# Optimization experiments

Measured on AMD Instinct MI355X. Metric: run time of the kernel, lower is better.

The kernel has to match this reference:

```python
import jax, jax.numpy as jnp
import numpy as np

ALPHA = 0.2  # LeakyReLU negative slope
NEG_BIG = -9e15


def setup_inputs() -> dict:
    key = jax.random.key(0)
    k_h, k_adj, k_W, k_a = jax.random.split(key, 4)
    B, N, F_in, F_out = 8, 2048, 128, 64
    h = jax.random.normal(k_h, (B, N, F_in), dtype=jnp.float32)
    adj = jax.random.randint(k_adj, (B, N, N), 0, 2, dtype=jnp.int32)
    # xavier_uniform: bound = sqrt(6/(fan_in+fan_out))
    bW = float(np.sqrt(6.0 / (F_in + F_out)))
    W = jax.random.uniform(k_W, (F_in, F_out), dtype=jnp.float32, minval=-bW, maxval=bW)
    ba = float(np.sqrt(6.0 / (2 * F_out + 1)))
    a = jax.random.uniform(k_a, (2 * F_out, 1), dtype=jnp.float32, minval=-ba, maxval=ba)
    return {"h": h, "adj": adj, "W": W, "a": a}


def reference(h, adj, W, a):
    # h: [B,N,Fin], adj: [B,N,N], W: [Fin,Fout], a: [2*Fout,1]
    F_out = W.shape[1]
    Wh = jnp.einsum('bnf,fo->bno', h, W)               # [B,N,Fout]
    a1 = a[:F_out, 0]                                   # [Fout] (source/i part)
    a2 = a[F_out:, 0]                                   # [Fout] (target/j part)
    # e_ij = leakyrelu(Wh_i . a1 + Wh_j . a2) -- avoids O(N^2*2F) concat
    si = Wh @ a1                                        # [B,N]
    sj = Wh @ a2                                        # [B,N]
    e = si[:, :, None] + sj[:, None, :]                 # [B,N,N]
    e = jnp.where(e > 0, e, ALPHA * e)                  # LeakyReLU
    e = jnp.where(adj > 0, e, NEG_BIG)                  # mask non-edges
    attention = jax.nn.softmax(e, axis=2)               # [B,N,N]
    # dropout omitted (eval / training=False)
    h_prime = jnp.einsum('bij,bjo->bio', attention, Wh)  # [B,N,Fout]
    return h_prime
```

## Files before the change

### kernel.cpp

```cpp
#include <hip/hip_runtime.h>
#include <hip/hip_bf16.h>

#define ALPHA 0.2f
#define LOG2E 1.4426950408889634f

typedef __attribute__((ext_vector_type(8))) short bf16x8;
typedef __attribute__((ext_vector_type(4))) float f32x4;
typedef __attribute__((ext_vector_type(4))) int i32x4;

__device__ __forceinline__ int cvt_pk_bf16(float lo, float hi) {
    int r;
    asm("v_cvt_pk_bf16_f32 %0, %1, %2" : "=v"(r) : "v"(lo), "v"(hi));
    return r;
}

__device__ __forceinline__ void stage16(const void* g, void* l) {
    __builtin_amdgcn_global_load_lds(
        (const __attribute__((address_space(1))) void*)g,
        (__attribute__((address_space(3))) void*)l, 16, 0, 0);
}

__global__ __launch_bounds__(256) void gat_precompute(
    const float* __restrict__ h, const float* __restrict__ W,
    const float* __restrict__ a, unsigned short* __restrict__ WhT,
    float* __restrict__ si2, float* __restrict__ sj2)
{
    __shared__ float h_lds[32][128];
    __shared__ float wh_lds[32][65];
    const int tid  = threadIdx.x;
    const int lane = tid & 63;
    const int wave = tid >> 6;
    const long long row0 = (long long)blockIdx.x * 32;

    {
        const float4* s4 = (const float4*)(h + row0 * 128);
        #pragma unroll
        for (int i = 0; i < 4; ++i) {
            int idx = tid + i * 256;
            float4 v = s4[idx];
            *(float4*)&h_lds[idx >> 5][(idx & 31) * 4] = v;
        }
    }
    __syncthreads();

    const float a1 = a[lane];
    const float a2 = a[64 + lane];
    float acc[8];
    #pragma unroll
    for (int r = 0; r < 8; ++r) acc[r] = 0.0f;

    for (int f = 0; f < 128; f += 4) {
        const float w0 = W[(f+0)*64 + lane];
        const float w1 = W[(f+1)*64 + lane];
        const float w2 = W[(f+2)*64 + lane];
        const float w3 = W[(f+3)*64 + lane];
        #pragma unroll
        for (int r = 0; r < 8; ++r) {
            const float4 hv = *(const float4*)&h_lds[wave*8 + r][f];
            acc[r] = fmaf(hv.x, w0, acc[r]);
            acc[r] = fmaf(hv.y, w1, acc[r]);
            acc[r] = fmaf(hv.z, w2, acc[r]);
            acc[r] = fmaf(hv.w, w3, acc[r]);
        }
    }

    #pragma unroll
    for (int r = 0; r < 8; ++r) {
        const int rr = wave*8 + r;
        wh_lds[rr][lane] = acc[r];
        float s1 = acc[r] * a1;
        float s2 = acc[r] * a2;
        #pragma unroll
        for (int off = 32; off > 0; off >>= 1) {
            s1 += __shfl_xor(s1, off);
            s2 += __shfl_xor(s2, off);
        }
        if (lane == 0) {
            si2[row0 + rr] = s1 * LOG2E;
            sj2[row0 + rr] = s2 * LOG2E;
        }
    }
    __syncthreads();

    const long long b  = row0 >> 11;
    const int n0 = (int)(row0 & 2047);
    const int o  = tid >> 2;
    const int c0 = (tid & 3) * 8;
    i32x4 pk;
    #pragma unroll
    for (int k = 0; k < 4; ++k)
        pk[k] = cvt_pk_bf16(wh_lds[c0 + 2*k][o], wh_lds[c0 + 2*k + 1][o]);
    *(i32x4*)(WhT + (b*64 + o)*2048 + n0 + c0) = pk;
}

__global__ __launch_bounds__(256) void gat_attention(
    const int* __restrict__ adj, const unsigned short* __restrict__ WhT,
    const float* __restrict__ si2, const float* __restrict__ sj2,
    float* __restrict__ out)
{
    __shared__ char ldsbuf[65536];
    const int tid  = threadIdx.x;
    const int lane = tid & 63;
    const int wave = tid >> 6;
    const int bid  = blockIdx.x;
    const int b    = bid >> 6;
    const int i0   = (bid & 63) << 5;
    const int arow = lane & 15;
    const int g    = lane >> 4;
    const int half = wave >> 1;
    const int rgrp = wave & 1;
    const long long bN = (long long)b * 2048;

    const int* asrc[4];
    #pragma unroll
    for (int rd = 0; rd < 4; ++rd) {
        int U = (wave*4 + rd)*64 + lane;
        int r = U >> 5, pu = U & 31;
        int u = pu ^ (r & 15);
        int col = (u < 16) ? u*4 : (1024 + (u-16)*4);
        asrc[rd] = adj + (bN + i0 + r)*2048 + col;
    }
    const unsigned short* wsrc[4];
    #pragma unroll
    for (int rd = 0; rd < 4; ++rd) {
        int U  = wave*256 + rd*64 + lane;
        int hf = U >> 9;
        int o  = (U & 511) >> 3;
        int pu = U & 7;
        wsrc[rd] = WhT + ((long long)b*64 + o)*2048 + hf*1024
                       + ((pu ^ (o & 7)) * 8);
    }

    const float* sjb = sj2 + bN;
    float mx = -INFINITY;
    #pragma unroll 4
    for (int i = 0; i < 32; ++i) mx = fmaxf(mx, sjb[lane + i*64]);
    #pragma unroll
    for (int off = 32; off > 0; off >>= 1) mx = fmaxf(mx, __shfl_xor(mx, off));

    const float si_r = si2[bN + i0 + rgrp*16 + arow];
    const float u0f  = si_r + mx;
    const float m2   = fmaxf(u0f, ALPHA * u0f);
    const float Ci   = si_r - m2;
    const float Di   = ALPHA * si_r - m2;
    const int   rr   = rgrp*16 + arow;

    f32x4 accf[4];
    #pragma unroll
    for (int ob = 0; ob < 4; ++ob) accf[ob] = (f32x4){0.f,0.f,0.f,0.f};
    f32x4 accl = (f32x4){0.f,0.f,0.f,0.f};
    bf16x8 ones;
    #pragma unroll
    for (int k = 0; k < 8; ++k) ones[k] = (short)0x3F80;

    #define STAGE(S, STEP) { \
        const int ja = (STEP) * 64; \
        char* ab_ = ldsbuf + (S)*32768; \
        stage16(asrc[0] + ja, ab_ + (wave*4+0)*1024); \
        stage16(asrc[1] + ja, ab_ + (wave*4+1)*1024); \
        stage16(asrc[2] + ja, ab_ + (wave*4+2)*1024); \
        stage16(asrc[3] + ja, ab_ + (wave*4+3)*1024); \
        char* wb_ = ldsbuf + (S)*32768 + 16384 + wave*4096; \
        stage16(wsrc[0] + ja, wb_ + 0*1024); \
        stage16(wsrc[1] + ja, wb_ + 1*1024); \
        stage16(wsrc[2] + ja, wb_ + 2*1024); \
        stage16(wsrc[3] + ja, wb_ + 3*1024); \
    }

    #define KKBODY(KK) { \
        const char* wb = ab + 16384 + half*8192; \
        const int ws = ((KK)*4 + g) ^ (arow & 7); \
        const bf16x8 bf0 = *(const bf16x8*)(wb + (( 0 + arow)*8 + ws)*16); \
        const bf16x8 bf1 = *(const bf16x8*)(wb + ((16 + arow)*8 + ws)*16); \
        const bf16x8 bf2 = *(const bf16x8*)(wb + ((32 + arow)*8 + ws)*16); \
        const bf16x8 bf3 = *(const bf16x8*)(wb + ((48 + arow)*8 + ws)*16); \
        const int u0a = half*16 + (KK)*8 + g*2; \
        const i32x4 A0 = *(const i32x4*)(ab + rr*512 + ((u0a    ) ^ arow)*16); \
        const i32x4 A1 = *(const i32x4*)(ab + rr*512 + ((u0a + 1) ^ arow)*16); \
        const float* sjp = sjb + half*1024 + j0 + (KK)*32 + g*8; \
        const f32x4 S0 = *(const f32x4*)(sjp); \
        const f32x4 S1 = *(const f32x4*)(sjp + 4); \
        float p[8]; \
        _Pragma("unroll") \
        for (int e = 0; e < 4; ++e) { \
            float pe = __builtin_amdgcn_exp2f( \
                fmaxf(Ci + S0[e], fmaf(ALPHA, S0[e], Di))); \
            p[e] = (A0[e] > 0) ? pe : 0.0f; \
        } \
        _Pragma("unroll") \
        for (int e = 0; e < 4; ++e) { \
            float pe = __builtin_amdgcn_exp2f( \
                fmaxf(Ci + S1[e], fmaf(ALPHA, S1[e], Di))); \
            p[4+e] = (A1[e] > 0) ? pe : 0.0f; \
        } \
        i32x4 pk_; \
        pk_[0] = cvt_pk_bf16(p[0], p[1]); \
        pk_[1] = cvt_pk_bf16(p[2], p[3]); \
        pk_[2] = cvt_pk_bf16(p[4], p[5]); \
        pk_[3] = cvt_pk_bf16(p[6], p[7]); \
        const bf16x8 pa = __builtin_bit_cast(bf16x8, pk_); \
        accl    = __builtin_amdgcn_mfma_f32_16x16x32_bf16(pa, ones, accl, 0, 0, 0); \
        accf[0] = __builtin_amdgcn_mfma_f32_16x16x32_bf16(pa, bf0, accf[0], 0, 0, 0); \
        accf[1] = __builtin_amdgcn_mfma_f32_16x16x32_bf16(pa, bf1, accf[1], 0, 0, 0); \
        accf[2] = __builtin_amdgcn_mfma_f32_16x16x32_bf16(pa, bf2, accf[2], 0, 0, 0); \
        accf[3] = __builtin_amdgcn_mfma_f32_16x16x32_bf16(pa, bf3, accf[3], 0, 0, 0); \
    }

    STAGE(0, 0);
    __syncthreads();

    int s = 0;
    for (int st = 0; st < 16; ++st) {
        if (st < 15) STAGE(s^1, st+1);
        const char* ab = ldsbuf + s*32768;
        const int j0 = st * 64;
        KKBODY(0);
        KKBODY(1);
        __syncthreads();
        s ^= 1;
    }

    float* accb = (float*)ldsbuf;
    float* lb   = (float*)(ldsbuf + 16384);
    #pragma unroll
    for (int ob = 0; ob < 4; ++ob)
        #pragma unroll
        for (int rg2 = 0; rg2 < 4; ++rg2)
            accb[(wave*16 + g*4 + rg2)*64 + ob*16 + arow] = accf[ob][rg2];
    if (arow == 0) {
        #pragma unroll
        for (int rg2 = 0; rg2 < 4; ++rg2)
            lb[wave*16 + g*4 + rg2] = accl[rg2];
    }
    __syncthreads();

    const int r  = tid >> 3;
    const int o0 = (tid & 7) * 8;
    const int rg = r >> 4, rl = r & 15;
    const float L   = lb[rg*16 + rl] + lb[(rg+2)*16 + rl];
    const float inv = 1.0f / L;
    float ov[8];
    #pragma unroll
    for (int k = 0; k < 8; ++k)
        ov[k] = (accb[(rg*16 + rl)*64 + o0 + k]
               + accb[((rg+2)*16 + rl)*64 + o0 + k]) * inv;
    float* op = out + (bN + i0 + r)*64 + o0;
    *(float4*)op       = (float4){ov[0], ov[1], ov[2], ov[3]};
    *(float4*)(op + 4) = (float4){ov[4], ov[5], ov[6], ov[7]};
}

extern "C" void kernel_launch(void* const* d_in, const int* in_sizes, int n_in,
                              void* d_out, int out_size, void* d_ws, size_t ws_size,
                              hipStream_t stream) {
    const float* h   = (const float*)d_in[0];
    const int*   adj = (const int*)d_in[1];
    const float* W   = (const float*)d_in[2];
    const float* a   = (const float*)d_in[3];
    float* out = (float*)d_out;

    unsigned short* WhT = (unsigned short*)d_ws;
    float* si2 = (float*)((char*)d_ws + (size_t)16384*64*2);
    float* sj2 = si2 + 16384;

    gat_precompute<<<512, 256, 0, stream>>>(h, W, a, WhT, si2, sj2);
    gat_attention<<<512, 256, 0, stream>>>(adj, WhT, si2, sj2, out);
}
```

Before: 48.24 us.

## Pack adjacency into bitmasks in a separate kernel before attention

Adds a gat_pack kernel that reads the int32 adjacency matrix once and ballots it into 64-bit masks. The attention kernel then loads one mask word per step instead of staging int32 adjacency tiles through LDS, which halves its LDS footprint and may allow higher occupancy. The full adjacency read still happens, now in a separate launch. That adds a kernel launch, a workspace write and re-read of the bitmask, and a pack kernel whose per-lane strided loads may coalesce poorly.

New measurement: 65.41 us. +35.6%, slower.

```diff
diff --git a/kernel.cpp b/kernel.cpp
--- a/kernel.cpp
+++ b/kernel.cpp
@@ -93,12 +93,38 @@
     *(i32x4*)(WhT + (b*64 + o)*2048 + n0 + c0) = pk;
 }
 
+__global__ __launch_bounds__(256) void gat_pack(
+    const int* __restrict__ adj, unsigned long long* __restrict__ pk)
+{
+    const int tid  = threadIdx.x;
+    const int lane = tid & 63;
+    const int wave = tid >> 6;
+    const int b    = blockIdx.x >> 6;
+    const int n0   = (blockIdx.x & 63) << 5;
+    const long long base = ((long long)b*2048 + n0) * 2048;
+
+    #pragma unroll
+    for (int gi = 0; gi < 8; ++gi) {
+        const int g = wave*8 + gi;
+        const int* src = adj + base + g*64 + lane;
+        unsigned long long mine = 0;
+        #pragma unroll 8
+        for (int r = 0; r < 32; ++r) {
+            const unsigned long long bal = __ballot(src[(long long)r*2048] > 0);
+            if (lane == r) mine = bal;
+        }
+        if (lane < 32)
+            pk[((long long)b*32 + g)*2048 + n0 + lane] = mine;
+    }
+}
+
 __global__ __launch_bounds__(256) void gat_attention(
-    const int* __restrict__ adj, const unsigned short* __restrict__ WhT,
+    const unsigned long long* __restrict__ pk,
+    const unsigned short* __restrict__ WhT,
     const float* __restrict__ si2, const float* __restrict__ sj2,
     float* __restrict__ out)
 {
-    __shared__ char ldsbuf[65536];
+    __shared__ char ldsbuf[33024];
     const int tid  = threadIdx.x;
     const int lane = tid & 63;
     const int wave = tid >> 6;
@@ -111,15 +137,6 @@
     const int rgrp = wave & 1;
     const long long bN = (long long)b * 2048;
 
-    const int* asrc[4];
-    #pragma unroll
-    for (int rd = 0; rd < 4; ++rd) {
-        int U = (wave*4 + rd)*64 + lane;
-        int r = U >> 5, pu = U & 31;
-        int u = pu ^ (r & 15);
-        int col = (u < 16) ? u*4 : (1024 + (u-16)*4);
-        asrc[rd] = adj + (bN + i0 + r)*2048 + col;
-    }
     const unsigned short* wsrc[4];
     #pragma unroll
     for (int rd = 0; rd < 4; ++rd) {
@@ -145,6 +162,9 @@
     const float Di   = ALPHA * si_r - m2;
     const int   rr   = rgrp*16 + arow;
 
+    const unsigned long long* pkb = pk + ((long long)b*32)*2048 + i0 + rr
+                                       + (long long)half*16*2048;
+
     f32x4 accf[4];
     #pragma unroll
     for (int ob = 0; ob < 4; ++ob) accf[ob] = (f32x4){0.f,0.f,0.f,0.f};
@@ -155,12 +175,7 @@
 
     #define STAGE(S, STEP) { \
         const int ja = (STEP) * 64; \
-        char* ab_ = ldsbuf + (S)*32768; \
-        stage16(asrc[0] + ja, ab_ + (wave*4+0)*1024); \
-        stage16(asrc[1] + ja, ab_ + (wave*4+1)*1024); \
-        stage16(asrc[2] + ja, ab_ + (wave*4+2)*1024); \
-        stage16(asrc[3] + ja, ab_ + (wave*4+3)*1024); \
-        char* wb_ = ldsbuf + (S)*32768 + 16384 + wave*4096; \
+        char* wb_ = ldsbuf + (S)*16384 + wave*4096; \
         stage16(wsrc[0] + ja, wb_ + 0*1024); \
         stage16(wsrc[1] + ja, wb_ + 1*1024); \
         stage16(wsrc[2] + ja, wb_ + 2*1024); \
@@ -168,15 +183,12 @@
     }
 
     #define KKBODY(KK) { \
-        const char* wb = ab + 16384 + half*8192; \
         const int ws = ((KK)*4 + g) ^ (arow & 7); \
-        const bf16x8 bf0 = *(const bf16x8*)(wb + (( 0 + arow)*8 + ws)*16); \
-        const bf16x8 bf1 = *(const bf16x8*)(wb + ((16 + arow)*8 + ws)*16); \
-        const bf16x8 bf2 = *(const bf16x8*)(wb + ((32 + arow)*8 + ws)*16); \
-        const bf16x8 bf3 = *(const bf16x8*)(wb + ((48 + arow)*8 + ws)*16); \
-        const int u0a = half*16 + (KK)*8 + g*2; \
-        const i32x4 A0 = *(const i32x4*)(ab + rr*512 + ((u0a    ) ^ arow)*16); \
-        const i32x4 A1 = *(const i32x4*)(ab + rr*512 + ((u0a + 1) ^ arow)*16); \
+        const bf16x8 bf0 = *(const bf16x8*)(wb0 + (( 0 + arow)*8 + ws)*16); \
+        const bf16x8 bf1 = *(const bf16x8*)(wb0 + ((16 + arow)*8 + ws)*16); \
+        const bf16x8 bf2 = *(const bf16x8*)(wb0 + ((32 + arow)*8 + ws)*16); \
+        const bf16x8 bf3 = *(const bf16x8*)(wb0 + ((48 + arow)*8 + ws)*16); \
+        const unsigned mb = ((unsigned)(bits >> ((KK)*32)) >> (g*8)) & 0xffu; \
         const float* sjp = sjb + half*1024 + j0 + (KK)*32 + g*8; \
         const f32x4 S0 = *(const f32x4*)(sjp); \
         const f32x4 S1 = *(const f32x4*)(sjp + 4); \
@@ -185,13 +197,13 @@
         for (int e = 0; e < 4; ++e) { \
             float pe = __builtin_amdgcn_exp2f( \
                 fmaxf(Ci + S0[e], fmaf(ALPHA, S0[e], Di))); \
-            p[e] = (A0[e] > 0) ? pe : 0.0f; \
+            p[e] = (mb & (1u << e)) ? pe : 0.0f; \
         } \
         _Pragma("unroll") \
         for (int e = 0; e < 4; ++e) { \
             float pe = __builtin_amdgcn_exp2f( \
                 fmaxf(Ci + S1[e], fmaf(ALPHA, S1[e], Di))); \
-            p[4+e] = (A1[e] > 0) ? pe : 0.0f; \
+            p[4+e] = (mb & (1u << (4+e))) ? pe : 0.0f; \
         } \
         i32x4 pk_; \
         pk_[0] = cvt_pk_bf16(p[0], p[1]); \
@@ -212,7 +224,8 @@
     int s = 0;
     for (int st = 0; st < 16; ++st) {
         if (st < 15) STAGE(s^1, st+1);
-        const char* ab = ldsbuf + s*32768;
+        const unsigned long long bits = pkb[(long long)st * 2048];
+        const char* wb0 = ldsbuf + s*16384 + half*8192;
         const int j0 = st * 64;
         KKBODY(0);
         KKBODY(1);
@@ -221,7 +234,7 @@
     }
 
     float* accb = (float*)ldsbuf;
-    float* lb   = (float*)(ldsbuf + 16384);
+    float* lb   = (float*)(ldsbuf + 32768);
     #pragma unroll
     for (int ob = 0; ob < 4; ++ob)
         #pragma unroll
@@ -261,7 +274,9 @@
     unsigned short* WhT = (unsigned short*)d_ws;
     float* si2 = (float*)((char*)d_ws + (size_t)16384*64*2);
     float* sj2 = si2 + 16384;
-
+    unsigned long long* pkb = (unsigned long long*)(sj2 + 16384);
+
+    gat_pack<<<512, 256, 0, stream>>>(adj, pkb);
     gat_precompute<<<512, 256, 0, stream>>>(h, W, a, WhT, si2, sj2);
-    gat_attention<<<512, 256, 0, stream>>>(adj, WhT, si2, sj2, out);
-}
+    gat_attention<<<512, 256, 0, stream>>>(pkb, WhT, si2, sj2, out);
+}
```

## Shrink attention tile to 16 rows and split output columns across waves

Applied to the files above, without the earlier changes.

The attention kernel now handles 16 query rows per block instead of 32 and launches 1024 blocks. Each wave computes half of the output columns, with K steps of 32 and a smaller double-buffered LDS footprint. Blocks are interleaved across batches. The aim is more blocks and more resident blocks per CU to hide latency on the adjacency stream, which dominates the work. The cost is that every wave now recomputes the exp/mask work, WhT tiles are reloaded per block (twice as often overall), and there are twice as many loop iterations and barriers.

After: 56.22 us. 16.5% more time.

```diff
diff --git a/kernel.cpp b/kernel.cpp
--- a/kernel.cpp
+++ b/kernel.cpp
@@ -98,37 +98,30 @@
     const float* __restrict__ si2, const float* __restrict__ sj2,
     float* __restrict__ out)
 {
-    __shared__ char ldsbuf[65536];
+    __shared__ char ldsbuf[24576];
     const int tid  = threadIdx.x;
     const int lane = tid & 63;
     const int wave = tid >> 6;
-    const int bid  = blockIdx.x;
-    const int b    = bid >> 6;
-    const int i0   = (bid & 63) << 5;
+    const int b    = blockIdx.x & 7;
+    const int i0   = (blockIdx.x >> 3) << 4;
     const int arow = lane & 15;
     const int g    = lane >> 4;
     const int half = wave >> 1;
-    const int rgrp = wave & 1;
+    const int os   = wave & 1;
     const long long bN = (long long)b * 2048;
 
-    const int* asrc[4];
-    #pragma unroll
-    for (int rd = 0; rd < 4; ++rd) {
-        int U = (wave*4 + rd)*64 + lane;
-        int r = U >> 5, pu = U & 31;
-        int u = pu ^ (r & 15);
-        int col = (u < 16) ? u*4 : (1024 + (u-16)*4);
-        asrc[rd] = adj + (bN + i0 + r)*2048 + col;
-    }
-    const unsigned short* wsrc[4];
-    #pragma unroll
-    for (int rd = 0; rd < 4; ++rd) {
-        int U  = wave*256 + rd*64 + lane;
-        int hf = U >> 9;
-        int o  = (U & 511) >> 3;
-        int pu = U & 7;
-        wsrc[rd] = WhT + ((long long)b*64 + o)*2048 + hf*1024
-                       + ((pu ^ (o & 7)) * 8);
+    const int r_  = (wave << 2) + (lane >> 4);
+    const int pu_ = lane & 15;
+    const int u_  = pu_ ^ r_;
+    const int* asrc = adj + (bN + i0 + r_)*2048 + (u_ >> 3)*1024 + (u_ & 7)*4;
+
+    const unsigned short* wsrc[2];
+    #pragma unroll
+    for (int k = 0; k < 2; ++k) {
+        int U = (wave*2 + k)*64 + lane;
+        int o = U >> 3, p = U & 7;
+        int l = p ^ (o & 7);
+        wsrc[k] = WhT + ((long long)b*64 + o)*2048 + (l >> 2)*1024 + (l & 3)*8;
     }
 
     const float* sjb = sj2 + bN;
@@ -138,115 +131,104 @@
     #pragma unroll
     for (int off = 32; off > 0; off >>= 1) mx = fmaxf(mx, __shfl_xor(mx, off));
 
-    const float si_r = si2[bN + i0 + rgrp*16 + arow];
+    const float si_r = si2[bN + i0 + arow];
     const float u0f  = si_r + mx;
     const float m2   = fmaxf(u0f, ALPHA * u0f);
     const float Ci   = si_r - m2;
     const float Di   = ALPHA * si_r - m2;
-    const int   rr   = rgrp*16 + arow;
-
-    f32x4 accf[4];
-    #pragma unroll
-    for (int ob = 0; ob < 4; ++ob) accf[ob] = (f32x4){0.f,0.f,0.f,0.f};
-    f32x4 accl = (f32x4){0.f,0.f,0.f,0.f};
+
+    f32x4 accf0 = (f32x4){0.f,0.f,0.f,0.f};
+    f32x4 accf1 = (f32x4){0.f,0.f,0.f,0.f};
+    f32x4 accl  = (f32x4){0.f,0.f,0.f,0.f};
     bf16x8 ones;
     #pragma unroll
     for (int k = 0; k < 8; ++k) ones[k] = (short)0x3F80;
 
     #define STAGE(S, STEP) { \
-        const int ja = (STEP) * 64; \
-        char* ab_ = ldsbuf + (S)*32768; \
-        stage16(asrc[0] + ja, ab_ + (wave*4+0)*1024); \
-        stage16(asrc[1] + ja, ab_ + (wave*4+1)*1024); \
-        stage16(asrc[2] + ja, ab_ + (wave*4+2)*1024); \
-        stage16(asrc[3] + ja, ab_ + (wave*4+3)*1024); \
-        char* wb_ = ldsbuf + (S)*32768 + 16384 + wave*4096; \
-        stage16(wsrc[0] + ja, wb_ + 0*1024); \
-        stage16(wsrc[1] + ja, wb_ + 1*1024); \
-        stage16(wsrc[2] + ja, wb_ + 2*1024); \
-        stage16(wsrc[3] + ja, wb_ + 3*1024); \
-    }
-
-    #define KKBODY(KK) { \
-        const char* wb = ab + 16384 + half*8192; \
-        const int ws = ((KK)*4 + g) ^ (arow & 7); \
-        const bf16x8 bf0 = *(const bf16x8*)(wb + (( 0 + arow)*8 + ws)*16); \
-        const bf16x8 bf1 = *(const bf16x8*)(wb + ((16 + arow)*8 + ws)*16); \
-        const bf16x8 bf2 = *(const bf16x8*)(wb + ((32 + arow)*8 + ws)*16); \
-        const bf16x8 bf3 = *(const bf16x8*)(wb + ((48 + arow)*8 + ws)*16); \
-        const int u0a = half*16 + (KK)*8 + g*2; \
-        const i32x4 A0 = *(const i32x4*)(ab + rr*512 + ((u0a    ) ^ arow)*16); \
-        const i32x4 A1 = *(const i32x4*)(ab + rr*512 + ((u0a + 1) ^ arow)*16); \
-        const float* sjp = sjb + half*1024 + j0 + (KK)*32 + g*8; \
-        const f32x4 S0 = *(const f32x4*)(sjp); \
-        const f32x4 S1 = *(const f32x4*)(sjp + 4); \
-        float p[8]; \
-        _Pragma("unroll") \
-        for (int e = 0; e < 4; ++e) { \
-            float pe = __builtin_amdgcn_exp2f( \
-                fmaxf(Ci + S0[e], fmaf(ALPHA, S0[e], Di))); \
-            p[e] = (A0[e] > 0) ? pe : 0.0f; \
-        } \
-        _Pragma("unroll") \
-        for (int e = 0; e < 4; ++e) { \
-            float pe = __builtin_amdgcn_exp2f( \
-                fmaxf(Ci + S1[e], fmaf(ALPHA, S1[e], Di))); \
-            p[4+e] = (A1[e] > 0) ? pe : 0.0f; \
-        } \
-        i32x4 pk_; \
-        pk_[0] = cvt_pk_bf16(p[0], p[1]); \
-        pk_[1] = cvt_pk_bf16(p[2], p[3]); \
-        pk_[2] = cvt_pk_bf16(p[4], p[5]); \
-        pk_[3] = cvt_pk_bf16(p[6], p[7]); \
-        const bf16x8 pa = __builtin_bit_cast(bf16x8, pk_); \
-        accl    = __builtin_amdgcn_mfma_f32_16x16x32_bf16(pa, ones, accl, 0, 0, 0); \
-        accf[0] = __builtin_amdgcn_mfma_f32_16x16x32_bf16(pa, bf0, accf[0], 0, 0, 0); \
-        accf[1] = __builtin_amdgcn_mfma_f32_16x16x32_bf16(pa, bf1, accf[1], 0, 0, 0); \
-        accf[2] = __builtin_amdgcn_mfma_f32_16x16x32_bf16(pa, bf2, accf[2], 0, 0, 0); \
-        accf[3] = __builtin_amdgcn_mfma_f32_16x16x32_bf16(pa, bf3, accf[3], 0, 0, 0); \
+        const int ja = (STEP) * 32; \
+        char* base = ldsbuf + (S)*12288; \
+        stage16(asrc + ja,     base + wave*1024); \
+        stage16(wsrc[0] + ja,  base + 4096 + wave*2048); \
+        stage16(wsrc[1] + ja,  base + 4096 + wave*2048 + 1024); \
     }
 
     STAGE(0, 0);
     __syncthreads();
 
     int s = 0;
-    for (int st = 0; st < 16; ++st) {
-        if (st < 15) STAGE(s^1, st+1);
-        const char* ab = ldsbuf + s*32768;
-        const int j0 = st * 64;
-        KKBODY(0);
-        KKBODY(1);
+    for (int st = 0; st < 32; ++st) {
+        if (st < 31) STAGE(s^1, st+1);
+        const char* ab = ldsbuf + s*12288;
+        const char* wb = ab + 4096;
+
+        const int o0 = os*32 + arow;
+        const int o1 = o0 + 16;
+        const int lu = half*4 + g;
+        const bf16x8 bf0 = *(const bf16x8*)(wb + o0*128 + (lu ^ (o0 & 7))*16);
+        const bf16x8 bf1 = *(const bf16x8*)(wb + o1*128 + (lu ^ (o1 & 7))*16);
+
+        const int ua = half*8 + g*2;
+        const i32x4 A0 = *(const i32x4*)(ab + arow*256 + ((ua    ) ^ arow)*16);
+        const i32x4 A1 = *(const i32x4*)(ab + arow*256 + ((ua + 1) ^ arow)*16);
+
+        const float* sjp = sjb + half*1024 + st*32 + g*8;
+        const f32x4 S0 = *(const f32x4*)(sjp);
+        const f32x4 S1 = *(const f32x4*)(sjp + 4);
+
+        float p[8];
+        #pragma unroll
+        for (int e = 0; e < 4; ++e) {
+            float pe = __builtin_amdgcn_exp2f(
+                fmaxf(Ci + S0[e], fmaf(ALPHA, S0[e], Di)));
+            p[e] = (A0[e] > 0) ? pe : 0.0f;
+        }
+        #pragma unroll
+        for (int e = 0; e < 4; ++e) {
+            float pe = __builtin_amdgcn_exp2f(
+                fmaxf(Ci + S1[e], fmaf(ALPHA, S1[e], Di)));
+            p[4+e] = (A1[e] > 0) ? pe : 0.0f;
+        }
+        i32x4 pk_;
+        pk_[0] = cvt_pk_bf16(p[0], p[1]);
+        pk_[1] = cvt_pk_bf16(p[2], p[3]);
+        pk_[2] = cvt_pk_bf16(p[4], p[5]);
+        pk_[3] = cvt_pk_bf16(p[6], p[7]);
+        const bf16x8 pa = __builtin_bit_cast(bf16x8, pk_);
+
+        if (os == 0)
+            accl = __builtin_amdgcn_mfma_f32_16x16x32_bf16(pa, ones, accl, 0, 0, 0);
+        accf0 = __builtin_amdgcn_mfma_f32_16x16x32_bf16(pa, bf0, accf0, 0, 0, 0);
+        accf1 = __builtin_amdgcn_mfma_f32_16x16x32_bf16(pa, bf1, accf1, 0, 0, 0);
+
         __syncthreads();
         s ^= 1;
     }
 
     float* accb = (float*)ldsbuf;
-    float* lb   = (float*)(ldsbuf + 16384);
-    #pragma unroll
-    for (int ob = 0; ob < 4; ++ob)
-        #pragma unroll
-        for (int rg2 = 0; rg2 < 4; ++rg2)
-            accb[(wave*16 + g*4 + rg2)*64 + ob*16 + arow] = accf[ob][rg2];
-    if (arow == 0) {
-        #pragma unroll
-        for (int rg2 = 0; rg2 < 4; ++rg2)
-            lb[wave*16 + g*4 + rg2] = accl[rg2];
-    }
-    __syncthreads();
-
-    const int r  = tid >> 3;
-    const int o0 = (tid & 7) * 8;
-    const int rg = r >> 4, rl = r & 15;
-    const float L   = lb[rg*16 + rl] + lb[(rg+2)*16 + rl];
+    float* lb   = (float*)(ldsbuf + 8192);
+    #pragma unroll
+    for (int reg = 0; reg < 4; ++reg) {
+        const int irow = g*4 + reg;
+        accb[(half*16 + irow)*64 + os*32 +      arow] = accf0[reg];
+        accb[(half*16 + irow)*64 + os*32 + 16 + arow] = accf1[reg];
+    }
+    if (os == 0 && arow == 0) {
+        #pragma unroll
+        for (int reg = 0; reg < 4; ++reg)
+            lb[half*16 + g*4 + reg] = accl[reg];
+    }
+    __syncthreads();
+
+    const int r  = tid >> 4;
+    const int c0 = (tid & 15) * 4;
+    const float L   = lb[r] + lb[16 + r];
     const float inv = 1.0f / L;
-    float ov[8];
-    #pragma unroll
-    for (int k = 0; k < 8; ++k)
-        ov[k] = (accb[(rg*16 + rl)*64 + o0 + k]
-               + accb[((rg+2)*16 + rl)*64 + o0 + k]) * inv;
-    float* op = out + (bN + i0 + r)*64 + o0;
-    *(float4*)op       = (float4){ov[0], ov[1], ov[2], ov[3]};
-    *(float4*)(op + 4) = (float4){ov[4], ov[5], ov[6], ov[7]};
+    float4 v;
+    v.x = (accb[r*64 + c0 + 0] + accb[(16 + r)*64 + c0 + 0]) * inv;
+    v.y = (accb[r*64 + c0 + 1] + accb[(16 + r)*64 + c0 + 1]) * inv;
+    v.z = (accb[r*64 + c0 + 2] + accb[(16 + r)*64 + c0 + 2]) * inv;
+    v.w = (accb[r*64 + c0 + 3] + accb[(16 + r)*64 + c0 + 3]) * inv;
+    *(float4*)(out + (bN + i0 + r)*64 + c0) = v;
 }
 
 extern "C" void kernel_launch(void* const* d_in, const int* in_sizes, int n_in,
@@ -263,5 +245,5 @@
     float* sj2 = si2 + 16384;
 
     gat_precompute<<<512, 256, 0, stream>>>(h, W, a, WhT, si2, sj2);
-    gat_attention<<<512, 256, 0, stream>>>(adj, WhT, si2, sj2, out);
-}
+    gat_attention<<<1024, 256, 0, stream>>>(adj, WhT, si2, sj2, out);
+}
```

## Stage tiles through registers instead of direct global-to-LDS loads; interleave batch in block index

Applied to the files above, without the earlier changes.

Replaces the asynchronous global_load_lds staging with ordinary vector global loads into registers, issued before the compute of the current tile and written to the alternate LDS buffer afterwards. This gives a register-prefetch double-buffer pipeline and peels the last iteration. It also remaps the block index so consecutive blocks cycle through batches rather than row tiles, which changes L2/cache locality of WhT and sj reads. The new scheme costs extra VGPRs and explicit LDS write instructions, which may reduce occupancy.

New measurement: 46.50 us. 3.6% less time.

```diff
diff --git a/kernel.cpp b/kernel.cpp
--- a/kernel.cpp
+++ b/kernel.cpp
@@ -12,12 +12,6 @@
     int r;
     asm("v_cvt_pk_bf16_f32 %0, %1, %2" : "=v"(r) : "v"(lo), "v"(hi));
     return r;
-}
-
-__device__ __forceinline__ void stage16(const void* g, void* l) {
-    __builtin_amdgcn_global_load_lds(
-        (const __attribute__((address_space(1))) void*)g,
-        (__attribute__((address_space(3))) void*)l, 16, 0, 0);
 }
 
 __global__ __launch_bounds__(256) void gat_precompute(
@@ -102,9 +96,8 @@
     const int tid  = threadIdx.x;
     const int lane = tid & 63;
     const int wave = tid >> 6;
-    const int bid  = blockIdx.x;
-    const int b    = bid >> 6;
-    const int i0   = (bid & 63) << 5;
+    const int b    = blockIdx.x & 7;
+    const int i0   = (int)((blockIdx.x >> 3) << 5);
     const int arow = lane & 15;
     const int g    = lane >> 4;
     const int half = wave >> 1;
@@ -153,18 +146,31 @@
     #pragma unroll
     for (int k = 0; k < 8; ++k) ones[k] = (short)0x3F80;
 
-    #define STAGE(S, STEP) { \
+    i32x4 a0_, a1_, a2_, a3_, w0_, w1_, w2_, w3_;
+
+    #define LOADREGS(STEP) { \
         const int ja = (STEP) * 64; \
-        char* ab_ = ldsbuf + (S)*32768; \
-        stage16(asrc[0] + ja, ab_ + (wave*4+0)*1024); \
-        stage16(asrc[1] + ja, ab_ + (wave*4+1)*1024); \
-        stage16(asrc[2] + ja, ab_ + (wave*4+2)*1024); \
-        stage16(asrc[3] + ja, ab_ + (wave*4+3)*1024); \
-        char* wb_ = ldsbuf + (S)*32768 + 16384 + wave*4096; \
-        stage16(wsrc[0] + ja, wb_ + 0*1024); \
-        stage16(wsrc[1] + ja, wb_ + 1*1024); \
-        stage16(wsrc[2] + ja, wb_ + 2*1024); \
-        stage16(wsrc[3] + ja, wb_ + 3*1024); \
+        a0_ = *(const i32x4*)(asrc[0] + ja); \
+        a1_ = *(const i32x4*)(asrc[1] + ja); \
+        a2_ = *(const i32x4*)(asrc[2] + ja); \
+        a3_ = *(const i32x4*)(asrc[3] + ja); \
+        w0_ = *(const i32x4*)(wsrc[0] + ja); \
+        w1_ = *(const i32x4*)(wsrc[1] + ja); \
+        w2_ = *(const i32x4*)(wsrc[2] + ja); \
+        w3_ = *(const i32x4*)(wsrc[3] + ja); \
+    }
+
+    #define WRITEREGS(S) { \
+        char* aw = ldsbuf + (S)*32768 + wave*4096 + lane*16; \
+        *(i32x4*)(aw)        = a0_; \
+        *(i32x4*)(aw + 1024) = a1_; \
+        *(i32x4*)(aw + 2048) = a2_; \
+        *(i32x4*)(aw + 3072) = a3_; \
+        char* ww = aw + 16384; \
+        *(i32x4*)(ww)        = w0_; \
+        *(i32x4*)(ww + 1024) = w1_; \
+        *(i32x4*)(ww + 2048) = w2_; \
+        *(i32x4*)(ww + 3072) = w3_; \
     }
 
     #define KKBODY(KK) { \
@@ -206,18 +212,26 @@
         accf[3] = __builtin_amdgcn_mfma_f32_16x16x32_bf16(pa, bf3, accf[3], 0, 0, 0); \
     }
 
-    STAGE(0, 0);
+    LOADREGS(0);
+    WRITEREGS(0);
     __syncthreads();
 
     int s = 0;
-    for (int st = 0; st < 16; ++st) {
-        if (st < 15) STAGE(s^1, st+1);
+    for (int st = 0; st < 15; ++st) {
+        LOADREGS(st + 1);
         const char* ab = ldsbuf + s*32768;
         const int j0 = st * 64;
         KKBODY(0);
         KKBODY(1);
+        WRITEREGS(s^1);
         __syncthreads();
         s ^= 1;
+    }
+    {
+        const char* ab = ldsbuf + s*32768;
+        const int j0 = 15 * 64;
+        KKBODY(0);
+        KKBODY(1);
     }
 
     float* accb = (float*)ldsbuf;
```
